# Optimization experiments

Measured on AMD Instinct MI355X. Metric: run time of the kernel, lower is better.

The kernel has to match this reference:

```python
import jax, jax.numpy as jnp
import numpy as np

N_NODES = 100000
N_EDGES = 1600000
F_IN = 512
HID = 128
N_CLASS = 6


def setup_inputs() -> dict:
    key = jax.random.key(0)
    ks = jax.random.split(key, 12)
    def unif(k, shape, stdv):
        return jax.random.uniform(k, shape, jnp.float32, -stdv, stdv)
    s1 = 1.0 / np.sqrt(HID); s4 = 1.0 / np.sqrt(N_CLASS)
    return {
        "x": jax.random.normal(ks[0], (N_NODES, F_IN), jnp.float32),
        "edge_row": jax.random.randint(ks[1], (N_EDGES,), 0, N_NODES, jnp.int32),
        "edge_col": jax.random.randint(ks[2], (N_EDGES,), 0, N_NODES, jnp.int32),
        "edge_weight": jax.random.uniform(ks[3], (N_EDGES,), jnp.float32),
        "W1": unif(ks[4], (F_IN, HID), s1), "b1": unif(ks[5], (HID,), s1),
        "W2": unif(ks[6], (HID, HID), s1), "b2": unif(ks[7], (HID,), s1),
        "W3": unif(ks[8], (HID, HID), s1), "b3": unif(ks[9], (HID,), s1),
        "W4": unif(ks[10], (HID, N_CLASS), s4), "b4": unif(ks[11], (N_CLASS,), s4),
    }


def _gcn_layer(x, row, col, w_e, W, b):
    # support = x @ W  (dense mm), then spmm(adj, support) in COO form:
    # out[i] = sum_{(i,j) in E} A[i,j] * support[j]
    support = x @ W                              # [N, F_out]
    msgs = support[col] * w_e[:, None]           # [E, F_out] gather + scale
    agg = jax.ops.segment_sum(msgs, row, num_segments=N_NODES)
    return agg + b


def reference(x, edge_row, edge_col, edge_weight, W1, b1, W2, b2, W3, b3, W4, b4):
    # eval mode: F.dropout(training=False) is identity
    h = jax.nn.relu(_gcn_layer(x, edge_row, edge_col, edge_weight, W1, b1))
    h = jax.nn.relu(_gcn_layer(h, edge_row, edge_col, edge_weight, W2, b2))
    h = jax.nn.relu(_gcn_layer(h, edge_row, edge_col, edge_weight, W3, b3))
    return _gcn_layer(h, edge_row, edge_col, edge_weight, W4, b4)
```

## Files before the change

kernel.cpp:

```cpp
#include <hip/hip_runtime.h>
#include <cstdint>

constexpr int NN = 100000;
constexpr int NE = 1600000;
constexpr int FIN = 512;
constexpr int HID = 128;
constexpr int NCLS = 6;
constexpr int EPAD = NE + 7 * NN;

typedef __attribute__((ext_vector_type(8))) short short8v;
typedef __attribute__((ext_vector_type(4))) float f32x4;

__device__ __forceinline__ unsigned short f2bf(float f) {
    uint32_t u = __float_as_uint(f);
    uint32_t r = u + 0x7FFFu + ((u >> 16) & 1u);
    return (unsigned short)(r >> 16);
}
__device__ __forceinline__ float bflo(uint32_t u) { return __uint_as_float(u << 16); }
__device__ __forceinline__ float bfhi(uint32_t u) { return __uint_as_float(u & 0xffff0000u); }

__device__ __forceinline__ void gl_lds16(const void* g, void* l) {
    __builtin_amdgcn_global_load_lds(
        (const __attribute__((address_space(1))) unsigned int*)(unsigned long long)g,
        (__attribute__((address_space(3))) unsigned int*)(unsigned int)(unsigned long long)l,
        16, 0, 0);
}

__global__ void cvt_w(const float* __restrict__ W, unsigned short* __restrict__ Bp, int K) {
    const int t = blockIdx.x * blockDim.x + threadIdx.x;
    const int total = (K / 32) * 8 * 64;
    if (t >= total) return;
    const int lane = t & 63;
    const int fi = t >> 6;
    const int n = fi & 7, ks = fi >> 3;
    const int krow = ks * 32 + (lane >> 4) * 8;
    const int col = n * 16 + (lane & 15);
    short8v sv;
    #pragma unroll
    for (int j = 0; j < 8; ++j) sv[j] = (short)f2bf(W[(size_t)(krow + j) * HID + col]);
    *(short8v*)&Bp[(size_t)t * 8] = sv;
}

template<int K, bool ABF>
__launch_bounds__(320)
__global__ void gemm_lds(const void* __restrict__ Av, const unsigned short* __restrict__ Bp,
                         unsigned short* __restrict__ C) {
    constexpr int BM    = 160;
    constexpr int KS    = 32;
    constexpr int EB    = ABF ? 2 : 4;
    constexpr int ROWB  = KS * EB;
    constexpr int SLOTS = ROWB / 16;
    constexpr int SMSK  = SLOTS - 1;
    constexpr int CHUNK = BM * ROWB;
    constexpr int WBYT  = CHUNK / 5;
    constexpr int NISS  = WBYT / 1024;
    constexpr int NS    = K / KS;

    __shared__ __attribute__((aligned(16))) unsigned char lds[2 * CHUNK];

    const int tid  = threadIdx.x;
    const int lane = tid & 63;
    const int wave = tid >> 6;
    const int row0 = blockIdx.x * BM;
    const int lr   = lane & 15;
    const int kg   = lane >> 4;

    const unsigned char* Ab = (const unsigned char*)Av;
    const size_t rowbytes = (size_t)K * EB;

    auto stage = [&](int bufsel, int ks) {
        const size_t kbyte = (size_t)ks * ROWB;
        #pragma unroll
        for (int i = 0; i < NISS; ++i) {
            const int Lw   = wave * WBYT + i * 1024 + lane * 16;
            const int row  = Lw / ROWB;
            const int slot = (Lw >> 4) & SMSK;
            const int src  = slot ^ (row & SMSK);
            const unsigned char* g = Ab + (size_t)(row0 + row) * rowbytes + kbyte + src * 16;
            void* l = (void*)&lds[bufsel * CHUNK + wave * WBYT + i * 1024];
            gl_lds16(g, l);
        }
    };

    f32x4 acc[2][8] = {};

    stage(0, 0);
    __syncthreads();

    int cur = 0;
    for (int ks = 0; ks < NS; ++ks) {
        if (ks + 1 < NS) stage(cur ^ 1, ks + 1);

        const unsigned char* base = &lds[cur * CHUNK];
        const int rA0 = wave * 32 + lr;
        const int rA1 = rA0 + 16;
        const int key = lr & SMSK;

        short8v a0, a1;
        if constexpr (ABF) {
            a0 = *(const short8v*)(base + rA0 * ROWB + ((kg ^ key) * 16));
            a1 = *(const short8v*)(base + rA1 * ROWB + ((kg ^ key) * 16));
        } else {
            const float4 f00 = *(const float4*)(base + rA0 * ROWB + (((2 * kg + 0) ^ key) * 16));
            const float4 f01 = *(const float4*)(base + rA0 * ROWB + (((2 * kg + 1) ^ key) * 16));
            const float4 f10 = *(const float4*)(base + rA1 * ROWB + (((2 * kg + 0) ^ key) * 16));
            const float4 f11 = *(const float4*)(base + rA1 * ROWB + (((2 * kg + 1) ^ key) * 16));
            a0[0] = (short)f2bf(f00.x); a0[1] = (short)f2bf(f00.y);
            a0[2] = (short)f2bf(f00.z); a0[3] = (short)f2bf(f00.w);
            a0[4] = (short)f2bf(f01.x); a0[5] = (short)f2bf(f01.y);
            a0[6] = (short)f2bf(f01.z); a0[7] = (short)f2bf(f01.w);
            a1[0] = (short)f2bf(f10.x); a1[1] = (short)f2bf(f10.y);
            a1[2] = (short)f2bf(f10.z); a1[3] = (short)f2bf(f10.w);
            a1[4] = (short)f2bf(f11.x); a1[5] = (short)f2bf(f11.y);
            a1[6] = (short)f2bf(f11.z); a1[7] = (short)f2bf(f11.w);
        }

        const unsigned short* bb = Bp + ((size_t)ks * 8 * 64 + lane) * 8;
        #pragma unroll
        for (int n = 0; n < 8; ++n) {
            const short8v b = *reinterpret_cast<const short8v*>(bb + (size_t)n * 64 * 8);
            acc[0][n] = __builtin_amdgcn_mfma_f32_16x16x32_bf16(a0, b, acc[0][n], 0, 0, 0);
            acc[1][n] = __builtin_amdgcn_mfma_f32_16x16x32_bf16(a1, b, acc[1][n], 0, 0, 0);
        }
        __syncthreads();
        cur ^= 1;
    }

    #pragma unroll
    for (int m = 0; m < 2; ++m)
        #pragma unroll
        for (int n = 0; n < 8; ++n)
            #pragma unroll
            for (int i = 0; i < 4; ++i) {
                const int r = row0 + wave * 32 + m * 16 + kg * 4 + i;
                C[(size_t)r * HID + n * 16 + lr] = f2bf(acc[m][n][i]);
            }
}

__global__ void gemm_w4(const unsigned short* __restrict__ H, const float* __restrict__ W,
                        float* __restrict__ S, int M) {
    __shared__ float Ws[HID * NCLS];
    for (int i = threadIdx.x; i < HID * NCLS; i += blockDim.x) Ws[i] = W[i];
    __syncthreads();
    const int r = blockIdx.x * blockDim.x + threadIdx.x;
    if (r >= M) return;
    float acc[NCLS] = {};
    const unsigned short* h = &H[(size_t)r * HID];
    for (int k0 = 0; k0 < HID; k0 += 8) {
        const uint4 hv = *reinterpret_cast<const uint4*>(&h[k0]);
        float hf[8];
        hf[0] = bflo(hv.x); hf[1] = bfhi(hv.x);
        hf[2] = bflo(hv.y); hf[3] = bfhi(hv.y);
        hf[4] = bflo(hv.z); hf[5] = bfhi(hv.z);
        hf[6] = bflo(hv.w); hf[7] = bfhi(hv.w);
        #pragma unroll
        for (int u = 0; u < 8; ++u)
            #pragma unroll
            for (int j = 0; j < NCLS; ++j)
                acc[j] = fmaf(hf[u], Ws[(k0 + u) * NCLS + j], acc[j]);
    }
    #pragma unroll
    for (int j = 0; j < NCLS; ++j) S[(size_t)r * NCLS + j] = acc[j];
}

__global__ void hist_k(const int* __restrict__ erow, int* __restrict__ cnt) {
    const int e = blockIdx.x * blockDim.x + threadIdx.x;
    if (e < NE) atomicAdd(&cnt[erow[e]], 1);
}

__global__ void scan1_k(const int* __restrict__ in, int* __restrict__ out,
                        int* __restrict__ bsum, int n) {
    __shared__ int s[256];
    const int tid = threadIdx.x;
    const int gid = blockIdx.x * 256 + tid;
    const int v = (gid < NN) ? ((in[gid] + 7) & ~7) : 0;
    s[tid] = v;
    __syncthreads();
    for (int off = 1; off < 256; off <<= 1) {
        const int t = (tid >= off) ? s[tid - off] : 0;
        __syncthreads();
        s[tid] += t;
        __syncthreads();
    }
    if (gid < n) out[gid] = s[tid] - v;
    if (tid == 255) bsum[blockIdx.x] = s[255];
}

__global__ void scan2_k(int* __restrict__ bsum, int nb) {
    __shared__ int s[512];
    const int tid = threadIdx.x;
    const int v = (tid < nb) ? bsum[tid] : 0;
    s[tid] = v;
    __syncthreads();
    for (int off = 1; off < 512; off <<= 1) {
        const int t = (tid >= off) ? s[tid - off] : 0;
        __syncthreads();
        s[tid] += t;
        __syncthreads();
    }
    if (tid < nb) bsum[tid] = s[tid] - v;
}

__global__ void scan3_k(int* __restrict__ out, const int* __restrict__ bsum, int n) {
    const int gid = blockIdx.x * 256 + threadIdx.x;
    if (gid < n) out[gid] += bsum[blockIdx.x];
}

__global__ void scatter_k(const int* __restrict__ erow, const int* __restrict__ ecol,
                          const float* __restrict__ ew,
                          const int* __restrict__ row_ptr, int* __restrict__ cur,
                          int2* __restrict__ edges) {
    const int e = blockIdx.x * blockDim.x + threadIdx.x;
    if (e >= NE) return;
    const int r = erow[e];
    const int pos = row_ptr[r] + atomicAdd(&cur[r], 1);
    edges[pos] = make_int2(ecol[e], __float_as_int(ew[e]));
}

template<bool RELU>
__launch_bounds__(256)
__global__ void spmm_bf16(const int* __restrict__ row_ptr,
                          const int2* __restrict__ edges,
                          const unsigned short* __restrict__ S,
                          const float* __restrict__ bias,
                          unsigned short* __restrict__ out) {
    const int lane = threadIdx.x & 63;
    const int row = blockIdx.x * 4 + (threadIdx.x >> 6);
    if (row >= NN) return;
    const int beg = row_ptr[row];
    const int end = row_ptr[row + 1];
    const int fo = lane * 2;
    float2 a0 = *reinterpret_cast<const float2*>(&bias[fo]);
    float2 a1 = {0.f, 0.f}, a2 = {0.f, 0.f}, a3 = {0.f, 0.f};

    for (int j = beg; j < end; j += 8) {
        const int4 p0 = *reinterpret_cast<const int4*>(edges + j);
        const int4 p1 = *reinterpret_cast<const int4*>(edges + j + 2);
        const int4 p2 = *reinterpret_cast<const int4*>(edges + j + 4);
        const int4 p3 = *reinterpret_cast<const int4*>(edges + j + 6);
        const uint32_t s0 = *reinterpret_cast<const uint32_t*>(&S[(size_t)p0.x * HID + fo]);
        const uint32_t s1 = *reinterpret_cast<const uint32_t*>(&S[(size_t)p0.z * HID + fo]);
        const uint32_t s2 = *reinterpret_cast<const uint32_t*>(&S[(size_t)p1.x * HID + fo]);
        const uint32_t s3 = *reinterpret_cast<const uint32_t*>(&S[(size_t)p1.z * HID + fo]);
        const uint32_t s4 = *reinterpret_cast<const uint32_t*>(&S[(size_t)p2.x * HID + fo]);
        const uint32_t s5 = *reinterpret_cast<const uint32_t*>(&S[(size_t)p2.z * HID + fo]);
        const uint32_t s6 = *reinterpret_cast<const uint32_t*>(&S[(size_t)p3.x * HID + fo]);
        const uint32_t s7 = *reinterpret_cast<const uint32_t*>(&S[(size_t)p3.z * HID + fo]);
        const float w0 = __int_as_float(p0.y), w1 = __int_as_float(p0.w);
        const float w2 = __int_as_float(p1.y), w3 = __int_as_float(p1.w);
        const float w4 = __int_as_float(p2.y), w5 = __int_as_float(p2.w);
        const float w6 = __int_as_float(p3.y), w7 = __int_as_float(p3.w);
        a0.x = fmaf(bflo(s0), w0, a0.x); a0.y = fmaf(bfhi(s0), w0, a0.y);
        a1.x = fmaf(bflo(s1), w1, a1.x); a1.y = fmaf(bfhi(s1), w1, a1.y);
        a2.x = fmaf(bflo(s2), w2, a2.x); a2.y = fmaf(bfhi(s2), w2, a2.y);
        a3.x = fmaf(bflo(s3), w3, a3.x); a3.y = fmaf(bfhi(s3), w3, a3.y);
        a0.x = fmaf(bflo(s4), w4, a0.x); a0.y = fmaf(bfhi(s4), w4, a0.y);
        a1.x = fmaf(bflo(s5), w5, a1.x); a1.y = fmaf(bfhi(s5), w5, a1.y);
        a2.x = fmaf(bflo(s6), w6, a2.x); a2.y = fmaf(bfhi(s6), w6, a2.y);
        a3.x = fmaf(bflo(s7), w7, a3.x); a3.y = fmaf(bfhi(s7), w7, a3.y);
    }
    float fx = (a0.x + a1.x) + (a2.x + a3.x);
    float fy = (a0.y + a1.y) + (a2.y + a3.y);
    if (RELU) { fx = fmaxf(fx, 0.f); fy = fmaxf(fy, 0.f); }
    const uint32_t o = (uint32_t)f2bf(fx) | ((uint32_t)f2bf(fy) << 16);
    *reinterpret_cast<uint32_t*>(&out[(size_t)row * HID + fo]) = o;
}

__launch_bounds__(256)
__global__ void spmm6(const int* __restrict__ row_ptr,
                      const int2* __restrict__ edges,
                      const float* __restrict__ S,
                      const float* __restrict__ bias,
                      float* __restrict__ out) {
    const int t = blockIdx.x * blockDim.x + threadIdx.x;
    const int row = t >> 4;
    const int sl = t & 15;
    if (row >= NN) return;
    const int beg = row_ptr[row];
    const int end = row_ptr[row + 1];
    float acc[NCLS] = {};
    for (int j = beg + sl; j < end; j += 16) {
        const int2 e = edges[j];
        const float w = __int_as_float(e.y);
        const float* s = &S[(size_t)e.x * NCLS];
        #pragma unroll
        for (int k = 0; k < NCLS; ++k) acc[k] = fmaf(s[k], w, acc[k]);
    }
    #pragma unroll
    for (int off = 8; off > 0; off >>= 1)
        #pragma unroll
        for (int k = 0; k < NCLS; ++k) acc[k] += __shfl_xor(acc[k], off, 64);
    if (sl == 0) {
        #pragma unroll
        for (int k = 0; k < NCLS; ++k) out[(size_t)row * NCLS + k] = acc[k] + bias[k];
    }
}

extern "C" void kernel_launch(void* const* d_in, const int* in_sizes, int n_in,
                              void* d_out, int out_size, void* d_ws, size_t ws_size,
                              hipStream_t stream) {
    const float* x    = (const float*)d_in[0];
    const int*   erow = (const int*)d_in[1];
    const int*   ecol = (const int*)d_in[2];
    const float* ew   = (const float*)d_in[3];
    const float* W1 = (const float*)d_in[4];  const float* b1 = (const float*)d_in[5];
    const float* W2 = (const float*)d_in[6];  const float* b2 = (const float*)d_in[7];
    const float* W3 = (const float*)d_in[8];  const float* b3 = (const float*)d_in[9];
    const float* W4 = (const float*)d_in[10]; const float* b4 = (const float*)d_in[11];
    float* out = (float*)d_out;

    int2*           edges_s = (int2*)d_ws;
    unsigned short* sup16   = (unsigned short*)(edges_s + EPAD);
    unsigned short* h16     = sup16 + (size_t)NN * HID;
    float*          sup6    = (float*)(h16 + (size_t)NN * HID);
    unsigned short* Bp1     = (unsigned short*)(sup6 + (size_t)NN * NCLS);
    unsigned short* Bp2     = Bp1 + (size_t)FIN * HID;
    unsigned short* Bp3     = Bp2 + (size_t)HID * HID;
    int*            row_ptr = (int*)(Bp3 + (size_t)HID * HID);
    int*            row_cnt = row_ptr + (NN + 1);
    int*            bsum    = row_cnt + NN;

    const dim3 blk(256);
    const int  g_edge = (NE + 255) / 256;
    const int  NB = (NN + 1 + 255) / 256;

    cvt_w<<<(FIN / 32 * 8 * 64 + 255) / 256, blk, 0, stream>>>(W1, Bp1, FIN);
    cvt_w<<<(HID / 32 * 8 * 64 + 255) / 256, blk, 0, stream>>>(W2, Bp2, HID);
    cvt_w<<<(HID / 32 * 8 * 64 + 255) / 256, blk, 0, stream>>>(W3, Bp3, HID);

    hipMemsetAsync(row_cnt, 0, (size_t)NN * sizeof(int), stream);
    hipMemsetAsync(edges_s, 0, (size_t)EPAD * sizeof(int2), stream);
    hist_k<<<g_edge, blk, 0, stream>>>(erow, row_cnt);
    scan1_k<<<NB, blk, 0, stream>>>(row_cnt, row_ptr, bsum, NN + 1);
    scan2_k<<<1, 512, 0, stream>>>(bsum, NB);
    scan3_k<<<NB, blk, 0, stream>>>(row_ptr, bsum, NN + 1);
    hipMemsetAsync(row_cnt, 0, (size_t)NN * sizeof(int), stream);
    scatter_k<<<g_edge, blk, 0, stream>>>(erow, ecol, ew, row_ptr, row_cnt, edges_s);

    const int g_gemm = NN / 160;
    const int g_spmm = NN / 4;

    gemm_lds<FIN, false><<<g_gemm, dim3(320), 0, stream>>>(x, Bp1, sup16);
    spmm_bf16<true><<<g_spmm, blk, 0, stream>>>(row_ptr, edges_s, sup16, b1, h16);
    gemm_lds<HID, true><<<g_gemm, dim3(320), 0, stream>>>(h16, Bp2, sup16);
    spmm_bf16<true><<<g_spmm, blk, 0, stream>>>(row_ptr, edges_s, sup16, b2, h16);
    gemm_lds<HID, true><<<g_gemm, dim3(320), 0, stream>>>(h16, Bp3, sup16);
    spmm_bf16<true><<<g_spmm, blk, 0, stream>>>(row_ptr, edges_s, sup16, b3, h16);
    gemm_w4<<<(NN + 255) / 256, blk, 0, stream>>>(h16, W4, sup6, NN);
    spmm6<<<(NN * 16 + 255) / 256, blk, 0, stream>>>(row_ptr, edges_s, sup6, b4, out);
}
```

Baseline: 495.2 us.

## Chunk support matrix by feature columns and pipeline GEMM B loads without block barriers

The GEMM now writes its output in a feature-chunked layout: eight 16-column slabs, each stored contiguously over all nodes. A new SpMM kernel assigns each block to one chunk and 32 rows, so every edge gather reads a 32-byte segment from a smaller working set, aiming for better cache locality. The GEMM preloads B fragments into registers and replaces __syncthreads with per-wave vmcnt waits, which relies on each wave staging only its own rows. Setup is also reduced: the three weight conversions become one launch, and a small pad kernel replaces the full memset of the edge array. In exchange, the edge list is read once per chunk (eight times per layer), and correctness depends on the wave-private LDS assumption.

```diff
diff --git a/kernel.cpp b/kernel.cpp
--- a/kernel.cpp
+++ b/kernel.cpp
@@ -26,10 +26,8 @@
         16, 0, 0);
 }
 
-__global__ void cvt_w(const float* __restrict__ W, unsigned short* __restrict__ Bp, int K) {
-    const int t = blockIdx.x * blockDim.x + threadIdx.x;
-    const int total = (K / 32) * 8 * 64;
-    if (t >= total) return;
+__device__ __forceinline__ void cvt_body(const float* __restrict__ W,
+                                         unsigned short* __restrict__ Bp, int t) {
     const int lane = t & 63;
     const int fi = t >> 6;
     const int n = fi & 7, ks = fi >> 3;
@@ -41,10 +39,22 @@
     *(short8v*)&Bp[(size_t)t * 8] = sv;
 }
 
+__global__ void cvt_w3(const float* __restrict__ W1, const float* __restrict__ W2,
+                       const float* __restrict__ W3,
+                       unsigned short* __restrict__ Bp1, unsigned short* __restrict__ Bp2,
+                       unsigned short* __restrict__ Bp3) {
+    const int t = blockIdx.x * blockDim.x + threadIdx.x;
+    constexpr int T1 = (FIN / 32) * 8 * 64;
+    constexpr int T2 = (HID / 32) * 8 * 64;
+    if (t < T1)                cvt_body(W1, Bp1, t);
+    else if (t < T1 + T2)      cvt_body(W2, Bp2, t - T1);
+    else if (t < T1 + 2 * T2)  cvt_body(W3, Bp3, t - T1 - T2);
+}
+
 template<int K, bool ABF>
 __launch_bounds__(320)
 __global__ void gemm_lds(const void* __restrict__ Av, const unsigned short* __restrict__ Bp,
-                         unsigned short* __restrict__ C) {
+                         unsigned short* __restrict__ Sc) {
     constexpr int BM    = 160;
     constexpr int KS    = 32;
     constexpr int EB    = ABF ? 2 : 4;
@@ -85,11 +95,22 @@
     f32x4 acc[2][8] = {};
 
     stage(0, 0);
-    __syncthreads();
 
     int cur = 0;
     for (int ks = 0; ks < NS; ++ks) {
-        if (ks + 1 < NS) stage(cur ^ 1, ks + 1);
+        short8v bfr[8];
+        const unsigned short* bb = Bp + ((size_t)ks * 8 * 64 + lane) * 8;
+        #pragma unroll
+        for (int n = 0; n < 8; ++n)
+            bfr[n] = *reinterpret_cast<const short8v*>(bb + (size_t)n * 64 * 8);
+
+        if (ks + 1 < NS) {
+            stage(cur ^ 1, ks + 1);
+            asm volatile("s_waitcnt vmcnt(%0)" :: "i"(NISS) : "memory");
+        } else {
+            asm volatile("s_waitcnt vmcnt(0)" ::: "memory");
+        }
+        __builtin_amdgcn_sched_barrier(0);
 
         const unsigned char* base = &lds[cur * CHUNK];
         const int rA0 = wave * 32 + lr;
@@ -115,14 +136,11 @@
             a1[6] = (short)f2bf(f11.z); a1[7] = (short)f2bf(f11.w);
         }
 
-        const unsigned short* bb = Bp + ((size_t)ks * 8 * 64 + lane) * 8;
         #pragma unroll
         for (int n = 0; n < 8; ++n) {
-            const short8v b = *reinterpret_cast<const short8v*>(bb + (size_t)n * 64 * 8);
-            acc[0][n] = __builtin_amdgcn_mfma_f32_16x16x32_bf16(a0, b, acc[0][n], 0, 0, 0);
-            acc[1][n] = __builtin_amdgcn_mfma_f32_16x16x32_bf16(a1, b, acc[1][n], 0, 0, 0);
+            acc[0][n] = __builtin_amdgcn_mfma_f32_16x16x32_bf16(a0, bfr[n], acc[0][n], 0, 0, 0);
+            acc[1][n] = __builtin_amdgcn_mfma_f32_16x16x32_bf16(a1, bfr[n], acc[1][n], 0, 0, 0);
         }
-        __syncthreads();
         cur ^= 1;
     }
 
@@ -133,7 +151,7 @@
             #pragma unroll
             for (int i = 0; i < 4; ++i) {
                 const int r = row0 + wave * 32 + m * 16 + kg * 4 + i;
-                C[(size_t)r * HID + n * 16 + lr] = f2bf(acc[m][n][i]);
+                Sc[((size_t)n * NN + r) * 16 + lr] = f2bf(acc[m][n][i]);
             }
 }
 
@@ -217,35 +235,47 @@
     edges[pos] = make_int2(ecol[e], __float_as_int(ew[e]));
 }
 
+__global__ void pad_k(const int* __restrict__ row_ptr, const int* __restrict__ cur,
+                      int2* __restrict__ edges) {
+    const int r = blockIdx.x * blockDim.x + threadIdx.x;
+    if (r >= NN) return;
+    const int end = row_ptr[r + 1];
+    for (int p = row_ptr[r] + cur[r]; p < end; ++p) edges[p] = make_int2(0, 0);
+}
+
 template<bool RELU>
 __launch_bounds__(256)
-__global__ void spmm_bf16(const int* __restrict__ row_ptr,
-                          const int2* __restrict__ edges,
-                          const unsigned short* __restrict__ S,
-                          const float* __restrict__ bias,
-                          unsigned short* __restrict__ out) {
-    const int lane = threadIdx.x & 63;
-    const int row = blockIdx.x * 4 + (threadIdx.x >> 6);
-    if (row >= NN) return;
+__global__ void spmm_l2(const int* __restrict__ row_ptr,
+                        const int2* __restrict__ edges,
+                        const unsigned short* __restrict__ Sc,
+                        const float* __restrict__ bias,
+                        unsigned short* __restrict__ out) {
+    const int chunk  = blockIdx.x & 7;
+    const int rowblk = blockIdx.x >> 3;
+    const int fl     = threadIdx.x & 7;
+    const int rowg   = threadIdx.x >> 3;
+    const int row    = rowblk * 32 + rowg;
     const int beg = row_ptr[row];
     const int end = row_ptr[row + 1];
-    const int fo = lane * 2;
-    float2 a0 = *reinterpret_cast<const float2*>(&bias[fo]);
-    float2 a1 = {0.f, 0.f}, a2 = {0.f, 0.f}, a3 = {0.f, 0.f};
+    const unsigned short* S = Sc + (size_t)chunk * NN * 16 + fl * 2;
+    const int f0 = chunk * 16 + fl * 2;
+
+    const float2 bv = *reinterpret_cast<const float2*>(&bias[f0]);
+    float2 a0 = bv, a1 = {0.f, 0.f}, a2 = {0.f, 0.f}, a3 = {0.f, 0.f};
 
     for (int j = beg; j < end; j += 8) {
         const int4 p0 = *reinterpret_cast<const int4*>(edges + j);
         const int4 p1 = *reinterpret_cast<const int4*>(edges + j + 2);
         const int4 p2 = *reinterpret_cast<const int4*>(edges + j + 4);
         const int4 p3 = *reinterpret_cast<const int4*>(edges + j + 6);
-        const uint32_t s0 = *reinterpret_cast<const uint32_t*>(&S[(size_t)p0.x * HID + fo]);
-        const uint32_t s1 = *reinterpret_cast<const uint32_t*>(&S[(size_t)p0.z * HID + fo]);
-        const uint32_t s2 = *reinterpret_cast<const uint32_t*>(&S[(size_t)p1.x * HID + fo]);
-        const uint32_t s3 = *reinterpret_cast<const uint32_t*>(&S[(size_t)p1.z * HID + fo]);
-        const uint32_t s4 = *reinterpret_cast<const uint32_t*>(&S[(size_t)p2.x * HID + fo]);
-        const uint32_t s5 = *reinterpret_cast<const uint32_t*>(&S[(size_t)p2.z * HID + fo]);
-        const uint32_t s6 = *reinterpret_cast<const uint32_t*>(&S[(size_t)p3.x * HID + fo]);
-        const uint32_t s7 = *reinterpret_cast<const uint32_t*>(&S[(size_t)p3.z * HID + fo]);
+        const uint32_t s0 = *reinterpret_cast<const uint32_t*>(&S[(size_t)p0.x * 16]);
+        const uint32_t s1 = *reinterpret_cast<const uint32_t*>(&S[(size_t)p0.z * 16]);
+        const uint32_t s2 = *reinterpret_cast<const uint32_t*>(&S[(size_t)p1.x * 16]);
+        const uint32_t s3 = *reinterpret_cast<const uint32_t*>(&S[(size_t)p1.z * 16]);
+        const uint32_t s4 = *reinterpret_cast<const uint32_t*>(&S[(size_t)p2.x * 16]);
+        const uint32_t s5 = *reinterpret_cast<const uint32_t*>(&S[(size_t)p2.z * 16]);
+        const uint32_t s6 = *reinterpret_cast<const uint32_t*>(&S[(size_t)p3.x * 16]);
+        const uint32_t s7 = *reinterpret_cast<const uint32_t*>(&S[(size_t)p3.z * 16]);
         const float w0 = __int_as_float(p0.y), w1 = __int_as_float(p0.w);
         const float w2 = __int_as_float(p1.y), w3 = __int_as_float(p1.w);
         const float w4 = __int_as_float(p2.y), w5 = __int_as_float(p2.w);
@@ -263,7 +293,7 @@
     float fy = (a0.y + a1.y) + (a2.y + a3.y);
     if (RELU) { fx = fmaxf(fx, 0.f); fy = fmaxf(fy, 0.f); }
     const uint32_t o = (uint32_t)f2bf(fx) | ((uint32_t)f2bf(fy) << 16);
-    *reinterpret_cast<uint32_t*>(&out[(size_t)row * HID + fo]) = o;
+    *reinterpret_cast<uint32_t*>(&out[(size_t)row * HID + f0]) = o;
 }
 
 __launch_bounds__(256)
@@ -318,34 +348,32 @@
     unsigned short* Bp3     = Bp2 + (size_t)HID * HID;
     int*            row_ptr = (int*)(Bp3 + (size_t)HID * HID);
     int*            row_cnt = row_ptr + (NN + 1);
-    int*            bsum    = row_cnt + NN;
+    int*            row_cur = row_cnt + NN;
+    int*            bsum    = row_cur + NN;
 
     const dim3 blk(256);
     const int  g_edge = (NE + 255) / 256;
     const int  NB = (NN + 1 + 255) / 256;
 
-    cvt_w<<<(FIN / 32 * 8 * 64 + 255) / 256, blk, 0, stream>>>(W1, Bp1, FIN);
-    cvt_w<<<(HID / 32 * 8 * 64 + 255) / 256, blk, 0, stream>>>(W2, Bp2, HID);
-    cvt_w<<<(HID / 32 * 8 * 64 + 255) / 256, blk, 0, stream>>>(W3, Bp3, HID);
-
-    hipMemsetAsync(row_cnt, 0, (size_t)NN * sizeof(int), stream);
-    hipMemsetAsync(edges_s, 0, (size_t)EPAD * sizeof(int2), stream);
+    cvt_w3<<<(12288 + 255) / 256, blk, 0, stream>>>(W1, W2, W3, Bp1, Bp2, Bp3);
+
+    hipMemsetAsync(row_cnt, 0, (size_t)2 * NN * sizeof(int), stream);
     hist_k<<<g_edge, blk, 0, stream>>>(erow, row_cnt);
     scan1_k<<<NB, blk, 0, stream>>>(row_cnt, row_ptr, bsum, NN + 1);
     scan2_k<<<1, 512, 0, stream>>>(bsum, NB);
     scan3_k<<<NB, blk, 0, stream>>>(row_ptr, bsum, NN + 1);
-    hipMemsetAsync(row_cnt, 0, (size_t)NN * sizeof(int), stream);
-    scatter_k<<<g_edge, blk, 0, stream>>>(erow, ecol, ew, row_ptr, row_cnt, edges_s);
+    scatter_k<<<g_edge, blk, 0, stream>>>(erow, ecol, ew, row_ptr, row_cur, edges_s);
+    pad_k<<<(NN + 255) / 256, blk, 0, stream>>>(row_ptr, row_cur, edges_s);
 
     const int g_gemm = NN / 160;
-    const int g_spmm = NN / 4;
+    const int g_spmm = 8 * (NN / 32);
 
     gemm_lds<FIN, false><<<g_gemm, dim3(320), 0, stream>>>(x, Bp1, sup16);
-    spmm_bf16<true><<<g_spmm, blk, 0, stream>>>(row_ptr, edges_s, sup16, b1, h16);
+    spmm_l2<true><<<g_spmm, blk, 0, stream>>>(row_ptr, edges_s, sup16, b1, h16);
     gemm_lds<HID, true><<<g_gemm, dim3(320), 0, stream>>>(h16, Bp2, sup16);
-    spmm_bf16<true><<<g_spmm, blk, 0, stream>>>(row_ptr, edges_s, sup16, b2, h16);
+    spmm_l2<true><<<g_spmm, blk, 0, stream>>>(row_ptr, edges_s, sup16, b2, h16);
     gemm_lds<HID, true><<<g_gemm, dim3(320), 0, stream>>>(h16, Bp3, sup16);
-    spmm_bf16<true><<<g_spmm, blk, 0, stream>>>(row_ptr, edges_s, sup16, b3, h16);
+    spmm_l2<true><<<g_spmm, blk, 0, stream>>>(row_ptr, edges_s, sup16, b3, h16);
     gemm_w4<<<(NN + 255) / 256, blk, 0, stream>>>(h16, W4, sup6, NN);
     spmm6<<<(NN * 16 + 255) / 256, blk, 0, stream>>>(row_ptr, edges_s, sup6, b4, out);
 }
```

Result: slower. 570.9 us (+15.3%).
